# Performance work log

Measured on AMD Instinct MI355X. Metric: run time of the kernel, lower is better.

The kernel has to match this reference:

```python
import jax, jax.numpy as jnp
import numpy as np

IN, H, OUT, T = 512, 2048, 512, 8192


def setup_inputs() -> dict:
    key = jax.random.key(0)
    ks = jax.random.split(key, 9)
    s = 1.0 / np.sqrt(H).astype(np.float32)  # PyTorch LSTM/Linear init range
    u = lambda k, shape: jax.random.uniform(k, shape, jnp.float32, -s, s)
    return {
        "sequence": jax.random.normal(ks[0], (T, IN), jnp.float32),
        "W_ih": u(ks[1], (4 * H, IN)),
        "W_hh": u(ks[2], (4 * H, H)),
        "b_ih": u(ks[3], (4 * H,)),
        "b_hh": u(ks[4], (4 * H,)),
        "h0": jax.random.normal(ks[5], (H,), jnp.float32),  # module's random hidden init (batch=1 flattened)
        "c0": jax.random.normal(ks[6], (H,), jnp.float32),
        "W_lin": u(ks[7], (OUT, H)),
        "b_lin": u(ks[8], (OUT,)),
    }


def reference(sequence, W_ih, W_hh, b_ih, b_hh, h0, c0, W_lin, b_lin):
    # Precompute input contribution to gates for all timesteps in one GEMM: [T, 4H]
    x_gates = sequence @ W_ih.T + (b_ih + b_hh)

    def cell(carry, xg):
        h, c = carry
        g = xg + h @ W_hh.T                      # [4H]
        i, f, gg, o = jnp.split(g, 4)            # PyTorch gate order: i, f, g, o
        i = jax.nn.sigmoid(i)
        f = jax.nn.sigmoid(f)
        gg = jnp.tanh(gg)
        o = jax.nn.sigmoid(o)
        c = f * c + i * gg
        h = o * jnp.tanh(c)
        return (h, c), h

    (h_last, _), _ = jax.lax.scan(cell, (h0, c0), x_gates)
    # linear on every step then take last == linear on last hidden state
    pred = h_last @ W_lin.T + b_lin              # [OUT]
    return pred[None, :]                          # [1, OUT], matches prediction[-1]
```

## Files before the change

### kernel.cpp

```cpp
#include <hip/hip_runtime.h>
#include <hip/hip_bf16.h>
#include <stdint.h>



__device__ __forceinline__ uint32_t packbf(float a, float b) {
    uint32_t ua = __float_as_uint(a);
    uint32_t ub = __float_as_uint(b);
    ua = (ua + 0x7fffu + ((ua >> 16) & 1u)) >> 16;
    ub = (ub + 0x7fffu + ((ub >> 16) & 1u)) >> 16;
    return ua | (ub << 16);
}

__device__ __forceinline__ float dot2bf(uint32_t a, uint32_t b, float c) {
    float d;
    asm("v_dot2_f32_bf16 %0, %1, %2, %3" : "=v"(d) : "v"(a), "v"(b), "v"(c));
    return d;
}

__device__ __forceinline__ float sigm(float x) { return 1.f / (1.f + __expf(-x)); }
__device__ __forceinline__ float tanh_fast(float x) { return 1.f - 2.f / (1.f + __expf(2.f * x)); }

#define ASTORE(p, v) __hip_atomic_store((p), (v), __ATOMIC_RELAXED, __HIP_MEMORY_SCOPE_AGENT)

__device__ __forceinline__ void aload_2x4(const unsigned long long* pa,
                                          const unsigned long long* pb,
                                          ulonglong2& ra, ulonglong2& rb) {
    asm volatile(
        "global_load_dwordx4 %0, %2, off sc0 sc1\n\t"
        "global_load_dwordx4 %1, %3, off sc0 sc1\n\t"
        "s_waitcnt vmcnt(0)"
        : "=v"(ra), "=v"(rb)
        : "v"(pa), "v"(pb)
        : "memory");
}

__global__ __launch_bounds__(256) void init_hbuf(unsigned long long* hbuf) {
    int i = blockIdx.x * 256 + threadIdx.x;
    if (i < 2048) hbuf[i] = ~0ull;
}

__global__ __launch_bounds__(256, 1) void lstm_persist(const float* __restrict__ seq,
                                                       const float* __restrict__ Wih,
                                                       const float* __restrict__ Whh,
                                                       const float* __restrict__ bih,
                                                       const float* __restrict__ bhh,
                                                       const float* __restrict__ h0,
                                                       const float* __restrict__ c0,
                                                       unsigned long long* hbuf,
                                                       float* __restrict__ hf32) {
    const int b = blockIdx.x, tid = threadIdx.x;
    const int q = tid >> 6, lane = tid & 63;
    const int hb = b * 8;
    const int rb = (lane >> 2) & 1;
    const int myrow = hb + 2 * q + rb;

    uint32_t w[160];
#pragma unroll
    for (int c = 0; c < 8; c++) {
        const int R = (c >> 1) * 2048 + hb + 2 * q + (c & 1);
        const float2* rih = (const float2*)(Wih + (size_t)R * 512);
        const float2* rhh = (const float2*)(Whh + (size_t)R * 2048);
#pragma unroll
        for (int k = 0; k < 4; k++) {
            float2 v = rih[k * 64 + lane];
            w[c * 20 + k] = packbf(v.x, v.y);
        }
#pragma unroll
        for (int k = 4; k < 20; k++) {
            float2 v = rhh[(k - 4) * 64 + lane];
            w[c * 20 + k] = packbf(v.x, v.y);
        }
    }

    __shared__ uint32_t v_stage[2][1024];

    const float bi  = bih[myrow] + bhh[myrow];
    const float bf_ = bih[2048 + myrow] + bhh[2048 + myrow];
    const float bg  = bih[4096 + myrow] + bhh[4096 + myrow];
    const float bo  = bih[6144 + myrow] + bhh[6144 + myrow];
    float c_state = c0[myrow];

    if (q == 0 && lane < 4) {
        float a = h0[hb + lane * 2], b2 = h0[hb + lane * 2 + 1];
        unsigned long long v = ((unsigned long long)packbf(a, b2) << 32);
        ASTORE(&hbuf[b * 4 + lane], v);
    }

    float2 xn[4];
#pragma unroll
    for (int k = 0; k < 4; k++) xn[k] = ((const float2*)seq)[k * 64 + lane];

    int gave_up = 0;

    for (int s = 1; s <= 8192; s++) {
        const int t = s - 1, bs = t & 1;
        const uint32_t want = (uint32_t)t;

        float acc[8];
        {
            uint32_t x0 = packbf(xn[0].x, xn[0].y), x1 = packbf(xn[1].x, xn[1].y);
            uint32_t x2 = packbf(xn[2].x, xn[2].y), x3 = packbf(xn[3].x, xn[3].y);
#pragma unroll
            for (int c = 0; c < 8; c++) {
                float a0 = dot2bf(w[c * 20 + 0], x0, 0.f);
                a0 = dot2bf(w[c * 20 + 1], x1, a0);
                a0 = dot2bf(w[c * 20 + 2], x2, a0);
                acc[c] = dot2bf(w[c * 20 + 3], x3, a0);
            }
        }
        if (s < 8192) {
            const float2* xp = (const float2*)(seq + (size_t)s * 512);
#pragma unroll
            for (int k = 0; k < 4; k++) xn[k] = xp[k * 64 + lane];
        }

        {
            const unsigned long long* base = hbuf + (bs << 10) + q * 256;
            const unsigned long long* pa = base + 2 * lane;
            const unsigned long long* pb = base + 128 + 2 * lane;
            ulonglong2 ra, rb2;
            if (!gave_up) {
                int tries = 0;
                for (;;) {
                    aload_2x4(pa, pb, ra, rb2);
                    int ok = ((uint32_t)ra.x == want) & ((uint32_t)ra.y == want) &
                             ((uint32_t)rb2.x == want) & ((uint32_t)rb2.y == want);
                    if (__all(ok)) break;
                    if (++tries > (1 << 17)) { gave_up = 1; break; }
                    if (tries > 1) __builtin_amdgcn_s_sleep(1);
                }
            } else {
                aload_2x4(pa, pb, ra, rb2);
            }
            uint2* vsa = (uint2*)&v_stage[bs][q * 256 + 2 * lane];
            uint2* vsb = (uint2*)&v_stage[bs][q * 256 + 128 + 2 * lane];
            *vsa = make_uint2((uint32_t)(ra.x >> 32), (uint32_t)(ra.y >> 32));
            *vsb = make_uint2((uint32_t)(rb2.x >> 32), (uint32_t)(rb2.y >> 32));
        }
        __syncthreads();

#pragma unroll
        for (int k = 0; k < 16; k++) {
            uint32_t hv = v_stage[bs][k * 64 + lane];
#pragma unroll
            for (int c = 0; c < 8; c++) acc[c] = dot2bf(w[c * 20 + 4 + k], hv, acc[c]);
        }

#pragma unroll
        for (int j = 0; j < 4; j++) {
            float lo = acc[j], hi = acc[j + 4];
            float sel = (lane & 1) ? lo : hi;
            float got = __shfl_xor(sel, 1, 64);
            acc[j] = ((lane & 1) ? hi : lo) + got;
        }
#pragma unroll
        for (int j = 0; j < 2; j++) {
            float lo = acc[j], hi = acc[j + 2];
            float sel = (lane & 2) ? lo : hi;
            float got = __shfl_xor(sel, 2, 64);
            acc[j] = ((lane & 2) ? hi : lo) + got;
        }
        {
            float lo = acc[0], hi = acc[1];
            float sel = (lane & 4) ? lo : hi;
            float got = __shfl_xor(sel, 4, 64);
            acc[0] = ((lane & 4) ? hi : lo) + got;
        }
        acc[0] += __shfl_xor(acc[0], 8, 64);
        acc[0] += __shfl_xor(acc[0], 16, 64);
        acc[0] += __shfl_xor(acc[0], 32, 64);

        const int base = lane & ~3;
        float gi = __shfl(acc[0], base, 64);
        float gg = __shfl(acc[0], base + 1, 64);
        float gf = __shfl(acc[0], base + 2, 64);
        float go = __shfl(acc[0], base + 3, 64);
        float i_ = sigm(gi + bi), f_ = sigm(gf + bf_), g_ = tanh_fast(gg + bg), o_ = sigm(go + bo);
        c_state = f_ * c_state + i_ * g_;
        float hval = o_ * tanh_fast(c_state);

        float h1 = __shfl(hval, 4, 64);
        if (lane == 0) {
            unsigned long long v = ((unsigned long long)packbf(hval, h1) << 32) | (uint32_t)s;
            ASTORE(&hbuf[((s & 1) << 10) + b * 4 + q], v);
            if (s == 8192) { hf32[hb + 2 * q] = hval; hf32[hb + 2 * q + 1] = h1; }
        }
    }
}

__global__ __launch_bounds__(256) void final_linear(const float* __restrict__ hf,
                                                    const float* __restrict__ Wlin,
                                                    const float* __restrict__ blin,
                                                    float* __restrict__ out) {
    const int row = blockIdx.x * 4 + (threadIdx.x >> 6);
    const int lane = threadIdx.x & 63;
    float acc = 0.f;
#pragma unroll
    for (int it = 0; it < 8; it++) {
        int c = it * 256 + lane * 4;
        float4 wv = *(const float4*)&Wlin[(size_t)row * 2048 + c];
        float4 hv = *(const float4*)&hf[c];
        acc += wv.x * hv.x + wv.y * hv.y + wv.z * hv.z + wv.w * hv.w;
    }
#pragma unroll
    for (int off = 32; off; off >>= 1) acc += __shfl_xor(acc, off, 64);
    if (lane == 0) out[row] = acc + blin[row];
}

extern "C" void kernel_launch(void* const* d_in, const int* in_sizes, int n_in,
                              void* d_out, int out_size, void* d_ws, size_t ws_size,
                              hipStream_t stream) {
    const float* seq  = (const float*)d_in[0];
    const float* Wih  = (const float*)d_in[1];
    const float* Whh  = (const float*)d_in[2];
    const float* bih  = (const float*)d_in[3];
    const float* bhh  = (const float*)d_in[4];
    const float* h0   = (const float*)d_in[5];
    const float* c0   = (const float*)d_in[6];
    const float* Wlin = (const float*)d_in[7];
    const float* blin = (const float*)d_in[8];
    float* out = (float*)d_out;

    char* ws = (char*)d_ws;
    unsigned long long* hbuf = (unsigned long long*)ws;
    float* hf32 = (float*)(ws + 16384);

    init_hbuf<<<8, 256, 0, stream>>>(hbuf);
    lstm_persist<<<256, 256, 0, stream>>>(seq, Wih, Whh, bih, bhh, h0, c0, hbuf, hf32);
    final_linear<<<128, 256, 0, stream>>>(hf32, Wlin, blin, out);
}
```

Before: 16.78 ms.

## Halve persistent LSTM grid by assigning 16 hidden units per block

```diff
diff --git a/kernel.cpp b/kernel.cpp
--- a/kernel.cpp
+++ b/kernel.cpp
@@ -51,14 +51,13 @@
                                                        float* __restrict__ hf32) {
     const int b = blockIdx.x, tid = threadIdx.x;
     const int q = tid >> 6, lane = tid & 63;
-    const int hb = b * 8;
-    const int rb = (lane >> 2) & 1;
-    const int myrow = hb + 2 * q + rb;
-
-    uint32_t w[160];
-#pragma unroll
-    for (int c = 0; c < 8; c++) {
-        const int R = (c >> 1) * 2048 + hb + 2 * q + (c & 1);
+    const int hb = b * 16;
+    const int myrow = hb + 4 * q + (lane & 3);
+
+    uint32_t w[320];
+#pragma unroll
+    for (int c = 0; c < 16; c++) {
+        const int R = (c >> 2) * 2048 + hb + 4 * q + (c & 3);
         const float2* rih = (const float2*)(Wih + (size_t)R * 512);
         const float2* rhh = (const float2*)(Whh + (size_t)R * 2048);
 #pragma unroll
@@ -81,10 +80,10 @@
     const float bo  = bih[6144 + myrow] + bhh[6144 + myrow];
     float c_state = c0[myrow];
 
-    if (q == 0 && lane < 4) {
-        float a = h0[hb + lane * 2], b2 = h0[hb + lane * 2 + 1];
+    if (q == 0 && lane < 8) {
+        float a = h0[hb + 2 * lane], b2 = h0[hb + 2 * lane + 1];
         unsigned long long v = ((unsigned long long)packbf(a, b2) << 32);
-        ASTORE(&hbuf[b * 4 + lane], v);
+        ASTORE(&hbuf[b * 8 + lane], v);
     }
 
     float2 xn[4];
@@ -97,12 +96,12 @@
         const int t = s - 1, bs = t & 1;
         const uint32_t want = (uint32_t)t;
 
-        float acc[8];
+        float acc[16];
         {
             uint32_t x0 = packbf(xn[0].x, xn[0].y), x1 = packbf(xn[1].x, xn[1].y);
             uint32_t x2 = packbf(xn[2].x, xn[2].y), x3 = packbf(xn[3].x, xn[3].y);
 #pragma unroll
-            for (int c = 0; c < 8; c++) {
+            for (int c = 0; c < 16; c++) {
                 float a0 = dot2bf(w[c * 20 + 0], x0, 0.f);
                 a0 = dot2bf(w[c * 20 + 1], x1, a0);
                 a0 = dot2bf(w[c * 20 + 2], x2, a0);
@@ -116,14 +115,12 @@
         }
 
         {
-            const unsigned long long* base = hbuf + (bs << 10) + q * 256;
-            const unsigned long long* pa = base + 2 * lane;
-            const unsigned long long* pb = base + 128 + 2 * lane;
+            const unsigned long long* base = hbuf + (bs << 10) + q * 256 + 4 * lane;
             ulonglong2 ra, rb2;
             if (!gave_up) {
                 int tries = 0;
                 for (;;) {
-                    aload_2x4(pa, pb, ra, rb2);
+                    aload_2x4(base, base + 2, ra, rb2);
                     int ok = ((uint32_t)ra.x == want) & ((uint32_t)ra.y == want) &
                              ((uint32_t)rb2.x == want) & ((uint32_t)rb2.y == want);
                     if (__all(ok)) break;
@@ -131,12 +128,11 @@
                     if (tries > 1) __builtin_amdgcn_s_sleep(1);
                 }
             } else {
-                aload_2x4(pa, pb, ra, rb2);
+                aload_2x4(base, base + 2, ra, rb2);
             }
-            uint2* vsa = (uint2*)&v_stage[bs][q * 256 + 2 * lane];
-            uint2* vsb = (uint2*)&v_stage[bs][q * 256 + 128 + 2 * lane];
-            *vsa = make_uint2((uint32_t)(ra.x >> 32), (uint32_t)(ra.y >> 32));
-            *vsb = make_uint2((uint32_t)(rb2.x >> 32), (uint32_t)(rb2.y >> 32));
+            *(uint4*)&v_stage[bs][q * 256 + 4 * lane] =
+                make_uint4((uint32_t)(ra.x >> 32), (uint32_t)(ra.y >> 32),
+                           (uint32_t)(rb2.x >> 32), (uint32_t)(rb2.y >> 32));
         }
         __syncthreads();
 
@@ -144,48 +140,56 @@
         for (int k = 0; k < 16; k++) {
             uint32_t hv = v_stage[bs][k * 64 + lane];
 #pragma unroll
-            for (int c = 0; c < 8; c++) acc[c] = dot2bf(w[c * 20 + 4 + k], hv, acc[c]);
-        }
-
-#pragma unroll
-        for (int j = 0; j < 4; j++) {
-            float lo = acc[j], hi = acc[j + 4];
+            for (int c = 0; c < 16; c++) acc[c] = dot2bf(w[c * 20 + 4 + k], hv, acc[c]);
+        }
+
+#pragma unroll
+        for (int j = 0; j < 8; j++) {
+            float lo = acc[j], hi = acc[j + 8];
             float sel = (lane & 1) ? lo : hi;
             float got = __shfl_xor(sel, 1, 64);
             acc[j] = ((lane & 1) ? hi : lo) + got;
         }
 #pragma unroll
-        for (int j = 0; j < 2; j++) {
-            float lo = acc[j], hi = acc[j + 2];
+        for (int j = 0; j < 4; j++) {
+            float lo = acc[j], hi = acc[j + 4];
             float sel = (lane & 2) ? lo : hi;
             float got = __shfl_xor(sel, 2, 64);
             acc[j] = ((lane & 2) ? hi : lo) + got;
         }
+#pragma unroll
+        for (int j = 0; j < 2; j++) {
+            float lo = acc[j], hi = acc[j + 2];
+            float sel = (lane & 4) ? lo : hi;
+            float got = __shfl_xor(sel, 4, 64);
+            acc[j] = ((lane & 4) ? hi : lo) + got;
+        }
         {
             float lo = acc[0], hi = acc[1];
-            float sel = (lane & 4) ? lo : hi;
-            float got = __shfl_xor(sel, 4, 64);
-            acc[0] = ((lane & 4) ? hi : lo) + got;
-        }
-        acc[0] += __shfl_xor(acc[0], 8, 64);
+            float sel = (lane & 8) ? lo : hi;
+            float got = __shfl_xor(sel, 8, 64);
+            acc[0] = ((lane & 8) ? hi : lo) + got;
+        }
         acc[0] += __shfl_xor(acc[0], 16, 64);
         acc[0] += __shfl_xor(acc[0], 32, 64);
 
-        const int base = lane & ~3;
-        float gi = __shfl(acc[0], base, 64);
-        float gg = __shfl(acc[0], base + 1, 64);
-        float gf = __shfl(acc[0], base + 2, 64);
-        float go = __shfl(acc[0], base + 3, 64);
+        const int base16 = lane & 48;
+        const int rr = ((lane & 1) << 3) | ((lane & 2) << 1);
+        float gi = __shfl(acc[0], base16 + rr, 64);
+        float gf = __shfl(acc[0], base16 + rr + 2, 64);
+        float gg = __shfl(acc[0], base16 + rr + 1, 64);
+        float go = __shfl(acc[0], base16 + rr + 3, 64);
         float i_ = sigm(gi + bi), f_ = sigm(gf + bf_), g_ = tanh_fast(gg + bg), o_ = sigm(go + bo);
         c_state = f_ * c_state + i_ * g_;
         float hval = o_ * tanh_fast(c_state);
 
-        float h1 = __shfl(hval, 4, 64);
-        if (lane == 0) {
-            unsigned long long v = ((unsigned long long)packbf(hval, h1) << 32) | (uint32_t)s;
-            ASTORE(&hbuf[((s & 1) << 10) + b * 4 + q], v);
-            if (s == 8192) { hf32[hb + 2 * q] = hval; hf32[hb + 2 * q + 1] = h1; }
-        }
+        float ha = __shfl(hval, 2 * (lane & 1), 64);
+        float hb2 = __shfl(hval, 2 * (lane & 1) + 1, 64);
+        if (lane < 2) {
+            unsigned long long v = ((unsigned long long)packbf(ha, hb2) << 32) | (uint32_t)s;
+            ASTORE(&hbuf[((s & 1) << 10) + b * 8 + 2 * q + lane], v);
+        }
+        if (s == 8192 && lane < 4) hf32[hb + 4 * q + lane] = hval;
     }
 }
 
@@ -227,6 +231,6 @@
     float* hf32 = (float*)(ws + 16384);
 
     init_hbuf<<<8, 256, 0, stream>>>(hbuf);
-    lstm_persist<<<256, 256, 0, stream>>>(seq, Wih, Whh, bih, bhh, h0, c0, hbuf, hf32);
+    lstm_persist<<<128, 256, 0, stream>>>(seq, Wih, Whh, bih, bhh, h0, c0, hbuf, hf32);
     final_linear<<<128, 256, 0, stream>>>(hf32, Wlin, blin, out);
 }
```

Measured after the change: 25.12 ms. 1.5x slower.
